# Kernel optimization log

Hardware: AMD Instinct MI355X
Metric: run time of the kernel (lower is better)

## Reference

```python
import jax, jax.numpy as jnp
import numpy as np


def _normalize_xyz_with_pc(pc, xyz):
    # Center by point-cloud centroid, scale by max radius of centered cloud.
    center = pc.mean(axis=1, keepdims=True)                      # [B,1,3]
    pc_c = pc - center
    scale = jnp.sqrt((pc_c ** 2).sum(-1)).max(axis=1)            # [B]
    scale = jnp.maximum(scale, 1e-6)[:, None, None]              # [B,1,1]
    return (xyz - center) / scale


def _nn_gather(seed_n, pts_n, feat):
    # seed_n [B,M,3], pts_n [B,K,3], feat [B,C,K] -> [B,C,M]
    d2 = ((seed_n ** 2).sum(-1)[:, :, None]
          + (pts_n ** 2).sum(-1)[:, None, :]
          - 2.0 * jnp.einsum('bmd,bkd->bmk', seed_n, pts_n))     # [B,M,K]
    idx = jnp.argmin(d2, axis=-1)                                # [B,M]
    return jnp.take_along_axis(feat, idx[:, None, :], axis=2)    # [B,C,M]


def _conv1x1(w, b, x):
    # w [O,C], b [O], x [B,C,M] -> [B,O,M]
    return jnp.einsum('oc,bcm->bom', w, x) + b[None, :, None]


def setup_inputs() -> dict:
    key = jax.random.key(0)
    ks = jax.random.split(key, 10)
    B, N, M, K, D = 4, 20000, 1024, 16384, 768
    return {
        'point_cloud': jax.random.normal(ks[0], (B, N, 3), jnp.float32),
        'seed_xyz': jax.random.normal(ks[1], (B, M, 3), jnp.float32),
        'seed_features': jax.random.normal(ks[2], (B, 256, M), jnp.float32),
        'pts': jax.random.normal(ks[3], (B, K, 3), jnp.float32),
        'feat': jax.random.normal(ks[4], (B, D, K), jnp.float32),
        'ln_gamma': jnp.ones((D,), jnp.float32),
        'ln_beta': jnp.zeros((D,), jnp.float32),
        'pw1': jax.random.normal(ks[5], (256, D), jnp.float32) * 0.02,
        'pb1': jnp.zeros((256,), jnp.float32),
        'pw2': jax.random.normal(ks[6], (256, 256), jnp.float32) * 0.02,
        'pb2': jnp.zeros((256,), jnp.float32),
        'fw1': jax.random.normal(ks[7], (256, 512), jnp.float32) * 0.02,
        'fb1': jnp.zeros((256,), jnp.float32),
        'fw2': jax.random.normal(ks[8], (256, 256), jnp.float32) * 0.02,
        'fb2': jnp.zeros((256,), jnp.float32),
    }


def reference(point_cloud, seed_xyz, seed_features, pts, feat,
              ln_gamma, ln_beta, pw1, pb1, pw2, pb2, fw1, fb1, fw2, fb2):
    seed_n = _normalize_xyz_with_pc(point_cloud, seed_xyz)       # [B,M,3]
    pts_n = _normalize_xyz_with_pc(point_cloud, pts)             # [B,K,3]
    vggt_raw = _nn_gather(seed_n, pts_n, feat)                   # [B,768,M]

    # LayerNorm over channel dim (applied on [B,M,768] in the original)
    x = vggt_raw.transpose(0, 2, 1)                              # [B,M,768]
    mu = x.mean(-1, keepdims=True)
    var = x.var(-1, keepdims=True)
    x_ln = ((x - mu) * jax.lax.rsqrt(var + 1e-5) * ln_gamma + ln_beta)
    x_ln = x_ln.transpose(0, 2, 1)                               # [B,768,M]

    vggt_proj = _conv1x1(pw2, pb2, jax.nn.relu(_conv1x1(pw1, pb1, x_ln)))
    fused = jnp.concatenate([seed_features, vggt_proj], axis=1)  # [B,512,M]
    mixed = _conv1x1(fw2, fb2, jax.nn.relu(_conv1x1(fw1, fb1, fused)))
    return mixed                                                 # [B,256,M]
```

## Files before the change

### kernel.cpp

```cpp
#include <hip/hip_runtime.h>
#include <math.h>

#define B_ 4
#define N_ 20000
#define M_ 1024
#define K_ 16384
#define D_ 768

typedef __attribute__((ext_vector_type(8))) short bf16x8;
typedef __attribute__((ext_vector_type(4))) float f32x4;

#define OFF_PART   0ul
#define OFF_RAD    1024ul
#define OFF_IDX    4096ul
#define OFF_P4     32768ul
#define OFF_NNP    1179648ul
#define OFF_G      2097152ul
#define OFF_XLN    16777216ul
#define OFF_FUSED  25165824ul
#define OFF_H2     29360128ul
#define OFF_WB1    33554432ul
#define OFF_WCAT   34603008ul
#define OFF_WB4    35651584ul
#define OFF_BC     36700160ul

__device__ inline unsigned short f2bf(float x) {
    union { float f; unsigned int u; } v; v.f = x;
    unsigned int r = v.u + 0x7fffu + ((v.u >> 16) & 1u);
    return (unsigned short)(r >> 16);
}

__device__ inline void gload_lds16(const void* g, void* lds) {
    __builtin_amdgcn_global_load_lds(
        (const __attribute__((address_space(1))) unsigned int*)g,
        (__attribute__((address_space(3))) unsigned int*)lds, 16, 0, 0);
}

__device__ inline void reduce_center(const float* part, int b,
                                     float& cx, float& cy, float& cz)
{
    cx = 0.f; cy = 0.f; cz = 0.f;
    #pragma unroll
    for (int r = 0; r < 16; ++r) {
        cx += part[(b*16+r)*3+0];
        cy += part[(b*16+r)*3+1];
        cz += part[(b*16+r)*3+2];
    }
    cx *= (1.f/N_); cy *= (1.f/N_); cz *= (1.f/N_);
}

__device__ inline float reduce_scale(const float* rad, int b)
{
    float m = 0.f;
    #pragma unroll
    for (int r = 0; r < 16; ++r) m = fmaxf(m, rad[b*16+r]);
    return fmaxf(sqrtf(m), 1e-6f);
}

__global__ __launch_bounds__(256) void k_pre(
    const float* __restrict__ pc,
    const float* __restrict__ pw1, const float* __restrict__ pw2,
    const float* __restrict__ pb2,
    const float* __restrict__ fw1, const float* __restrict__ fb1,
    const float* __restrict__ fw2,
    unsigned short* __restrict__ Wb1, unsigned short* __restrict__ Wcat,
    unsigned short* __restrict__ Wb4, float* __restrict__ bc,
    float* __restrict__ part)
{
    int bid = blockIdx.x, t = threadIdx.x;
    int lane = t & 63, wv = t >> 6;
    __shared__ float red[3][4];

    if (bid < 768) {
        int i0 = bid*256 + t;
        Wb1[i0] = f2bf(pw1[i0]);
        if (i0 < 65536) {
            int o = i0 >> 8, c = i0 & 255;
            Wcat[(size_t)o*512 + c] = f2bf(fw1[(size_t)o*512 + c]);
            Wb4[i0] = f2bf(fw2[i0]);
        }
    }
    if (bid < 256) {
        const float* fb = fw1 + (size_t)bid*512 + 256;
        float acc = 0.f;
        for (int j = 0; j < 256; ++j)
            acc = fmaf(fb[j], pw2[j*256 + t], acc);
        Wcat[(size_t)bid*512 + 256 + t] = f2bf(acc);
        float v = fb[t] * pb2[t];
        for (int off = 32; off; off >>= 1) v += __shfl_down(v, off, 64);
        if (!lane) red[0][wv] = v;
        __syncthreads();
        if (!t) bc[bid] = red[0][0]+red[0][1]+red[0][2]+red[0][3] + fb1[bid];
    } else if (bid >= 768) {
        int pi = bid - 768;
        int b = pi >> 4, chunk = pi & 15;
        const float* p = pc + (size_t)b * N_ * 3;
        int i0 = chunk * 1250;
        float sx = 0.f, sy = 0.f, sz = 0.f;
        for (int i = i0 + t; i < i0 + 1250; i += 256) {
            sx += p[i*3+0]; sy += p[i*3+1]; sz += p[i*3+2];
        }
        for (int off = 32; off; off >>= 1) {
            sx += __shfl_down(sx, off, 64);
            sy += __shfl_down(sy, off, 64);
            sz += __shfl_down(sz, off, 64);
        }
        if (!lane) { red[0][wv] = sx; red[1][wv] = sy; red[2][wv] = sz; }
        __syncthreads();
        if (!t) {
            part[(b*16+chunk)*3+0] = red[0][0]+red[0][1]+red[0][2]+red[0][3];
            part[(b*16+chunk)*3+1] = red[1][0]+red[1][1]+red[1][2]+red[1][3];
            part[(b*16+chunk)*3+2] = red[2][0]+red[2][1]+red[2][2]+red[2][3];
        }
    }
}

__global__ __launch_bounds__(256) void k_cs_rad(const float* __restrict__ pc,
                                                const float* __restrict__ part,
                                                float* __restrict__ rad)
{
    int blk = blockIdx.x, b = blk >> 4, pi = blk & 15;
    float cx, cy, cz;
    reduce_center(part, b, cx, cy, cz);
    const float* p = pc + (size_t)b * N_ * 3;
    int tid = threadIdx.x;
    int i0 = pi * 1250;
    float mx = 0.f;
    for (int i = i0 + tid; i < i0 + 1250; i += 256) {
        float dx = p[i*3+0]-cx, dy = p[i*3+1]-cy, dz = p[i*3+2]-cz;
        mx = fmaxf(mx, dx*dx + dy*dy + dz*dz);
    }
    for (int off = 32; off; off >>= 1) mx = fmaxf(mx, __shfl_down(mx, off, 64));
    __shared__ float red[4];
    int w = tid >> 6, l = tid & 63;
    if (!l) red[w] = mx;
    __syncthreads();
    if (!tid) rad[b*16+pi] = fmaxf(fmaxf(red[0], red[1]), fmaxf(red[2], red[3]));
}

__global__ __launch_bounds__(256) void k_prep_pts(const float* __restrict__ pts,
                                                  const float* __restrict__ part,
                                                  const float* __restrict__ rad,
                                                  float4* __restrict__ P4)
{
    int blk = blockIdx.x, b = blk >> 6;
    float cx, cy, cz;
    reduce_center(part, b, cx, cy, cz);
    float sc = 1.f / reduce_scale(rad, b);
    int k = (blk & 63)*256 + threadIdx.x;
    const float* pp = pts + ((size_t)b*K_ + k)*3;
    float px = (pp[0]-cx)*sc, py = (pp[1]-cy)*sc, pz = (pp[2]-cz)*sc;
    P4[(size_t)b*K_ + k] = make_float4(px, py, pz, px*px + py*py + pz*pz);
}

__global__ __launch_bounds__(256) void k_nn_part(const float* __restrict__ seed_xyz,
                                                 const float4* __restrict__ P4,
                                                 const float* __restrict__ part,
                                                 const float* __restrict__ rad,
                                                 float2* __restrict__ nnp)
{
    int blk = blockIdx.x;
    int ks = blk & 3, g = (blk >> 2) & 127, b = blk >> 9;
    float cx, cy, cz;
    reduce_center(part, b, cx, cy, cz);
    float scinv = 1.f / reduce_scale(rad, b);
    int t = threadIdx.x;
    int j = t & 31, s = t >> 5;
    int m = g*8 + s;
    const float* sp = seed_xyz + ((size_t)b*M_ + m)*3;
    float sx = (sp[0]-cx)*scinv, sy = (sp[1]-cy)*scinv, sz = (sp[2]-cz)*scinv;
    float ssq = sx*sx + sy*sy + sz*sz;
    const float4* Pb = P4 + (size_t)b*K_ + ks*4096;

    float best[4] = {3.4e38f, 3.4e38f, 3.4e38f, 3.4e38f};
    int   bk[4]   = {0, 0, 0, 0};
    for (int i = 0; i < 128; i += 4) {
        #pragma unroll
        for (int r = 0; r < 4; ++r) {
            int kk = (i + r)*32 + j;
            float4 q = Pb[kk];
            float d2 = ssq + q.w - 2.f*(sx*q.x + sy*q.y + sz*q.z);
            if (d2 < best[r]) { best[r] = d2; bk[r] = kk; }
        }
    }
    float bm = best[0]; int bmk = bk[0];
    #pragma unroll
    for (int r = 1; r < 4; ++r)
        if (best[r] < bm || (best[r] == bm && bk[r] < bmk)) { bm = best[r]; bmk = bk[r]; }
    #pragma unroll
    for (int mask = 16; mask; mask >>= 1) {
        float ob = __shfl_xor(bm, mask, 64);
        int   ok = __shfl_xor(bmk, mask, 64);
        if (ob < bm || (ob == bm && ok < bmk)) { bm = ob; bmk = ok; }
    }
    if (j == 0)
        nnp[((size_t)(b*M_ + m) << 2) + ks] = make_float2(bm, __int_as_float(ks*4096 + bmk));
}

__global__ __launch_bounds__(256) void k_nn_reduce(const float2* __restrict__ nnp,
                                                   int* __restrict__ idx)
{
    int i = blockIdx.x*256 + threadIdx.x;
    float bm = 3.4e38f; int bmk = 0;
    bool first = true;
    #pragma unroll
    for (int r = 0; r < 4; ++r) {
        float2 v = nnp[((size_t)i << 2) + r];
        int k = __float_as_int(v.y);
        if (first || v.x < bm || (v.x == bm && k < bmk)) { bm = v.x; bmk = k; first = false; }
    }
    idx[i] = bmk;
}

__global__ __launch_bounds__(256) void k_gather_tsf(const float* __restrict__ feat,
                                                    const int* __restrict__ idx,
                                                    const float* __restrict__ sf,
                                                    float* __restrict__ G,
                                                    unsigned short* __restrict__ fused)
{
    int bid = blockIdx.x, t = threadIdx.x;
    if (bid < 3072) {
        int b = bid / 768, c = bid - b*768;
        const float* frow = feat + ((size_t)b*D_ + c) * K_;
        const int* ib = idx + b*M_;
        float* grow = G + ((size_t)b*D_ + c) * M_;
        #pragma unroll
        for (int r = 0; r < 4; ++r) {
            int m = r*256 + t;
            grow[m] = frow[ib[m]];
        }
    } else {
        __shared__ float tile[32][33];
        int id = bid - 3072;
        int b = id >> 8, rem = id & 255;
        int m0 = (rem & 31) * 32, c0 = (rem >> 5) * 32;
        int tx = t & 31, ty = t >> 5;
        #pragma unroll
        for (int rr = 0; rr < 32; rr += 8)
            tile[ty+rr][tx] = sf[((size_t)b*256 + c0+ty+rr)*M_ + m0 + tx];
        __syncthreads();
        #pragma unroll
        for (int rr = 0; rr < 32; rr += 8)
            fused[((size_t)(b*M_ + m0+ty+rr))*512 + c0 + tx] = f2bf(tile[tx][ty+rr]);
    }
}

__global__ __launch_bounds__(256) void k_ln_fused(const float* __restrict__ G,
                                                  const float* __restrict__ gamma,
                                                  const float* __restrict__ beta,
                                                  unsigned short* __restrict__ xln)
{
    int b = blockIdx.y, m0 = blockIdx.x * 32;
    int t = threadIdx.x;
    int ml = t & 31, cp = t >> 5;
    const float* Gb = G + (size_t)b * D_ * M_;
    float s = 0.f, q = 0.f;
    for (int c = cp; c < D_; c += 8) {
        float v = Gb[(size_t)c*M_ + m0 + ml];
        s += v; q += v*v;
    }
    __shared__ float sred[8][32], qred[8][32];
    __shared__ float mu[32], iv[32];
    sred[cp][ml] = s; qred[cp][ml] = q;
    __syncthreads();
    if (t < 32) {
        float S = 0.f, Q = 0.f;
        #pragma unroll
        for (int r = 0; r < 8; ++r) { S += sred[r][t]; Q += qred[r][t]; }
        float m_ = S * (1.f/768.f);
        mu[t] = m_;
        iv[t] = rsqrtf(Q * (1.f/768.f) - m_*m_ + 1e-5f);
    }
    __syncthreads();

    __shared__ float tile[64][33];
    int ty = t >> 5;
    int cx2 = t & 31;
    for (int c0 = 0; c0 < D_; c0 += 64) {
        __syncthreads();
        #pragma unroll
        for (int ri = 0; ri < 8; ++ri) {
            int cl = ty*8 + ri;
            tile[cl][ml] = Gb[(size_t)(c0+cl)*M_ + m0 + ml];
        }
        __syncthreads();
        float2 ga = *(const float2*)&gamma[c0 + 2*cx2];
        float2 be = *(const float2*)&beta[c0 + 2*cx2];
        #pragma unroll
        for (int ri = 0; ri < 4; ++ri) {
            int m_l = ty*4 + ri;
            float v0 = (tile[2*cx2+0][m_l] - mu[m_l]) * iv[m_l] * ga.x + be.x;
            float v1 = (tile[2*cx2+1][m_l] - mu[m_l]) * iv[m_l] * ga.y + be.y;
            ushort2 pk = make_ushort2(f2bf(v0), f2bf(v1));
            *(ushort2*)&xln[((size_t)((b<<10) + m0 + m_l))*D_ + c0 + 2*cx2] = pk;
        }
    }
}

__global__ __launch_bounds__(256) void k_gemm_mfma(
    const unsigned short* __restrict__ X, const unsigned short* __restrict__ W,
    const float* __restrict__ bias, int Kdim, int relu, int mode,
    unsigned short* __restrict__ Ybf, int rowStride, int colOff,
    float* __restrict__ Yf)
{
    __shared__ unsigned short Al[64*64];
    __shared__ unsigned short Wl[64*64];
    int t = threadIdx.x, l = t & 63, w = t >> 6;
    int m0 = blockIdx.x * 64, o0 = blockIdx.y * 64;
    f32x4 acc[4];
    #pragma unroll
    for (int j = 0; j < 4; ++j) acc[j] = (f32x4){0.f, 0.f, 0.f, 0.f};

    for (int kc = 0; kc < Kdim; kc += 64) {
        #pragma unroll
        for (int i = 0; i < 2; ++i) {
            int lin = i*4096 + w*1024;
            int lb  = lin + l*16;
            int row = lb >> 7;
            int k16 = (lb >> 4) & 7;
            int ks  = k16 ^ (row & 7);
            gload_lds16(X + (size_t)(m0+row)*Kdim + kc + ks*8, (char*)Al + lin);
            gload_lds16(W + (size_t)(o0+row)*Kdim + kc + ks*8, (char*)Wl + lin);
        }
        __syncthreads();
        #pragma unroll
        for (int kk = 0; kk < 2; ++kk) {
            int arow = w*16 + (l & 15);
            int h = l >> 4;
            bf16x8 a = *(const bf16x8*)&Al[arow*64 + (((kk<<2)|h) ^ (arow & 7))*8];
            #pragma unroll
            for (int j = 0; j < 4; ++j) {
                int orow = j*16 + (l & 15);
                bf16x8 bfr = *(const bf16x8*)&Wl[orow*64 + (((kk<<2)|h) ^ (orow & 7))*8];
                acc[j] = __builtin_amdgcn_mfma_f32_16x16x32_bf16(a, bfr, acc[j], 0, 0, 0);
            }
        }
        __syncthreads();
    }

    int mbase = m0 + w*16 + (l >> 4)*4;
    if (mode == 0) {
        #pragma unroll
        for (int j = 0; j < 4; ++j) {
            int o = o0 + j*16 + (l & 15);
            float bi = bias[o];
            #pragma unroll
            for (int r = 0; r < 4; ++r) {
                float v = acc[j][r] + bi;
                if (relu) v = fmaxf(v, 0.f);
                Ybf[(size_t)(mbase + r)*rowStride + colOff + o] = f2bf(v);
            }
        }
    } else {
        int b = mbase >> 10, ml = mbase & 1023;
        #pragma unroll
        for (int j = 0; j < 4; ++j) {
            int o = o0 + j*16 + (l & 15);
            float bi = bias[o];
            float4 sv = make_float4(acc[j][0]+bi, acc[j][1]+bi, acc[j][2]+bi, acc[j][3]+bi);
            *(float4*)&Yf[((size_t)(b*256 + o))*1024 + ml] = sv;
        }
    }
}

extern "C" void kernel_launch(void* const* d_in, const int* in_sizes, int n_in,
                              void* d_out, int out_size, void* d_ws, size_t ws_size,
                              hipStream_t stream)
{
    (void)in_sizes; (void)n_in; (void)out_size; (void)ws_size;
    const float* pc        = (const float*)d_in[0];
    const float* seed_xyz  = (const float*)d_in[1];
    const float* seed_feat = (const float*)d_in[2];
    const float* pts       = (const float*)d_in[3];
    const float* feat      = (const float*)d_in[4];
    const float* ln_g      = (const float*)d_in[5];
    const float* ln_b      = (const float*)d_in[6];
    const float* pw1       = (const float*)d_in[7];
    const float* pb1       = (const float*)d_in[8];
    const float* pw2       = (const float*)d_in[9];
    const float* pb2       = (const float*)d_in[10];
    const float* fw1       = (const float*)d_in[11];
    const float* fb1       = (const float*)d_in[12];
    const float* fw2       = (const float*)d_in[13];
    const float* fb2       = (const float*)d_in[14];
    float* out = (float*)d_out;

    char* ws = (char*)d_ws;
    float*          part  = (float*)(ws + OFF_PART);
    float*          rad   = (float*)(ws + OFF_RAD);
    int*            idx   = (int*)(ws + OFF_IDX);
    float4*         P4    = (float4*)(ws + OFF_P4);
    float2*         nnp   = (float2*)(ws + OFF_NNP);
    float*          G     = (float*)(ws + OFF_G);
    unsigned short* xln   = (unsigned short*)(ws + OFF_XLN);
    unsigned short* fused = (unsigned short*)(ws + OFF_FUSED);
    unsigned short* h2    = (unsigned short*)(ws + OFF_H2);
    unsigned short* Wb1   = (unsigned short*)(ws + OFF_WB1);
    unsigned short* Wcat  = (unsigned short*)(ws + OFF_WCAT);
    unsigned short* Wb4   = (unsigned short*)(ws + OFF_WB4);
    float*          bc    = (float*)(ws + OFF_BC);

    k_pre<<<832, 256, 0, stream>>>(pc, pw1, pw2, pb2, fw1, fb1, fw2,
                                   Wb1, Wcat, Wb4, bc, part);
    k_cs_rad<<<64, 256, 0, stream>>>(pc, part, rad);
    k_prep_pts<<<256, 256, 0, stream>>>(pts, part, rad, P4);
    k_nn_part<<<2048, 256, 0, stream>>>(seed_xyz, P4, part, rad, nnp);
    k_nn_reduce<<<16, 256, 0, stream>>>(nnp, idx);
    k_gather_tsf<<<4096, 256, 0, stream>>>(feat, idx, seed_feat, G, fused);
    k_ln_fused<<<dim3(M_/32, B_), 256, 0, stream>>>(G, ln_g, ln_b, xln);
    k_gemm_mfma<<<dim3(64, 4), 256, 0, stream>>>(xln, Wb1, pb1, 768, 1, 0, fused, 512, 256, nullptr);
    k_gemm_mfma<<<dim3(64, 4), 256, 0, stream>>>(fused, Wcat, bc, 512, 1, 0, h2, 256, 0, nullptr);
    k_gemm_mfma<<<dim3(64, 4), 256, 0, stream>>>(h2, Wb4, fb2, 256, 0, 1, nullptr, 0, 0, out);
}
```

Before: 147.9 us.

## Double-buffer LDS tiles in MFMA GEMM and gather two channels per block

The GEMM kernel now keeps two LDS buffers and prefetches the next K-tile while computing on the current one, hiding global-to-LDS load latency. The gather kernel processes two feature channels per block, reusing the loaded indices and issuing more independent loads per thread, with the grid shrunk accordingly. This doubles LDS use in the GEMM, which may reduce occupancy.

```diff
diff --git a/kernel.cpp b/kernel.cpp
--- a/kernel.cpp
+++ b/kernel.cpp
@@ -219,19 +219,29 @@
                                                     unsigned short* __restrict__ fused)
 {
     int bid = blockIdx.x, t = threadIdx.x;
-    if (bid < 3072) {
-        int b = bid / 768, c = bid - b*768;
-        const float* frow = feat + ((size_t)b*D_ + c) * K_;
+    if (bid < 1536) {
+        int b = bid / 384;
+        int c = (bid - b*384) * 2;
+        const float* frow0 = feat + ((size_t)b*D_ + c) * K_;
+        const float* frow1 = frow0 + K_;
         const int* ib = idx + b*M_;
-        float* grow = G + ((size_t)b*D_ + c) * M_;
-        #pragma unroll
-        for (int r = 0; r < 4; ++r) {
-            int m = r*256 + t;
-            grow[m] = frow[ib[m]];
-        }
+        float* g0 = G + ((size_t)b*D_ + c) * M_;
+        float* g1 = g0 + M_;
+        int id4[4];
+        #pragma unroll
+        for (int r = 0; r < 4; ++r) id4[r] = ib[r*256 + t];
+        float v0[4], v1[4];
+        #pragma unroll
+        for (int r = 0; r < 4; ++r) v0[r] = frow0[id4[r]];
+        #pragma unroll
+        for (int r = 0; r < 4; ++r) v1[r] = frow1[id4[r]];
+        #pragma unroll
+        for (int r = 0; r < 4; ++r) g0[r*256 + t] = v0[r];
+        #pragma unroll
+        for (int r = 0; r < 4; ++r) g1[r*256 + t] = v1[r];
     } else {
         __shared__ float tile[32][33];
-        int id = bid - 3072;
+        int id = bid - 1536;
         int b = id >> 8, rem = id & 255;
         int m0 = (rem & 31) * 32, c0 = (rem >> 5) * 32;
         int tx = t & 31, ty = t >> 5;
@@ -303,35 +313,49 @@
     unsigned short* __restrict__ Ybf, int rowStride, int colOff,
     float* __restrict__ Yf)
 {
-    __shared__ unsigned short Al[64*64];
-    __shared__ unsigned short Wl[64*64];
+    __shared__ unsigned short Al[2][64*64];
+    __shared__ unsigned short Wl[2][64*64];
     int t = threadIdx.x, l = t & 63, w = t >> 6;
     int m0 = blockIdx.x * 64, o0 = blockIdx.y * 64;
     f32x4 acc[4];
     #pragma unroll
     for (int j = 0; j < 4; ++j) acc[j] = (f32x4){0.f, 0.f, 0.f, 0.f};
 
-    for (int kc = 0; kc < Kdim; kc += 64) {
-        #pragma unroll
-        for (int i = 0; i < 2; ++i) {
-            int lin = i*4096 + w*1024;
-            int lb  = lin + l*16;
-            int row = lb >> 7;
-            int k16 = (lb >> 4) & 7;
-            int ks  = k16 ^ (row & 7);
-            gload_lds16(X + (size_t)(m0+row)*Kdim + kc + ks*8, (char*)Al + lin);
-            gload_lds16(W + (size_t)(o0+row)*Kdim + kc + ks*8, (char*)Wl + lin);
-        }
-        __syncthreads();
+    int lin0 = w*1024;
+    int lb0  = lin0 + l*16;
+    int row0 = lb0 >> 7;
+    int ks0  = ((lb0 >> 4) & 7) ^ (row0 & 7);
+    int lin1 = 4096 + w*1024;
+    int lb1  = lin1 + l*16;
+    int row1 = lb1 >> 7;
+    int ks1  = ((lb1 >> 4) & 7) ^ (row1 & 7);
+
+    int nt = Kdim >> 6;
+
+    gload_lds16(X + (size_t)(m0+row0)*Kdim + ks0*8, (char*)&Al[0][0] + lin0);
+    gload_lds16(W + (size_t)(o0+row0)*Kdim + ks0*8, (char*)&Wl[0][0] + lin0);
+    gload_lds16(X + (size_t)(m0+row1)*Kdim + ks1*8, (char*)&Al[0][0] + lin1);
+    gload_lds16(W + (size_t)(o0+row1)*Kdim + ks1*8, (char*)&Wl[0][0] + lin1);
+    __syncthreads();
+
+    for (int tt = 0; tt < nt; ++tt) {
+        int cur = tt & 1;
+        if (tt + 1 < nt) {
+            int kc = (tt + 1) << 6;
+            gload_lds16(X + (size_t)(m0+row0)*Kdim + kc + ks0*8, (char*)&Al[cur^1][0] + lin0);
+            gload_lds16(W + (size_t)(o0+row0)*Kdim + kc + ks0*8, (char*)&Wl[cur^1][0] + lin0);
+            gload_lds16(X + (size_t)(m0+row1)*Kdim + kc + ks1*8, (char*)&Al[cur^1][0] + lin1);
+            gload_lds16(W + (size_t)(o0+row1)*Kdim + kc + ks1*8, (char*)&Wl[cur^1][0] + lin1);
+        }
         #pragma unroll
         for (int kk = 0; kk < 2; ++kk) {
             int arow = w*16 + (l & 15);
             int h = l >> 4;
-            bf16x8 a = *(const bf16x8*)&Al[arow*64 + (((kk<<2)|h) ^ (arow & 7))*8];
+            bf16x8 a = *(const bf16x8*)&Al[cur][arow*64 + (((kk<<2)|h) ^ (arow & 7))*8];
             #pragma unroll
             for (int j = 0; j < 4; ++j) {
                 int orow = j*16 + (l & 15);
-                bf16x8 bfr = *(const bf16x8*)&Wl[orow*64 + (((kk<<2)|h) ^ (orow & 7))*8];
+                bf16x8 bfr = *(const bf16x8*)&Wl[cur][orow*64 + (((kk<<2)|h) ^ (orow & 7))*8];
                 acc[j] = __builtin_amdgcn_mfma_f32_16x16x32_bf16(a, bfr, acc[j], 0, 0, 0);
             }
         }
@@ -406,7 +430,7 @@
     k_prep_pts<<<256, 256, 0, stream>>>(pts, part, rad, P4);
     k_nn_part<<<2048, 256, 0, stream>>>(seed_xyz, P4, part, rad, nnp);
     k_nn_reduce<<<16, 256, 0, stream>>>(nnp, idx);
-    k_gather_tsf<<<4096, 256, 0, stream>>>(feat, idx, seed_feat, G, fused);
+    k_gather_tsf<<<2560, 256, 0, stream>>>(feat, idx, seed_feat, G, fused);
     k_ln_fused<<<dim3(M_/32, B_), 256, 0, stream>>>(G, ln_g, ln_b, xln);
     k_gemm_mfma<<<dim3(64, 4), 256, 0, stream>>>(xln, Wb1, pb1, 768, 1, 0, fused, 512, 256, nullptr);
     k_gemm_mfma<<<dim3(64, 4), 256, 0, stream>>>(fused, Wcat, bc, 512, 1, 0, h2, 256, 0, nullptr);
```

Result: faster. 143.3 us, median of 2 (-3.1%).
